# Optimization experiments

Hardware: AMD Instinct MI355X
Metric: run time of the kernel (lower is better)

## Reference

```python
import jax, jax.numpy as jnp
import numpy as np

NX, NY, NZ = 256, 256, 64
M = 400000
NFEATS = 16
OFFSETS = [(dx, dy, dz) for dx in (-1, 0, 1) for dy in (-1, 0, 1) for dz in (-1, 0, 1)]


def setup_inputs() -> dict:
    key = jax.random.key(0)
    ks = jax.random.split(key, 24)
    # unique active voxel sites (submanifold conv assumes unique active coords)
    flat = jax.random.permutation(ks[0], NX * NY * NZ)[:M]
    x = (flat // (NY * NZ)).astype(jnp.int32)
    y = ((flat // NZ) % NY).astype(jnp.int32)
    z = (flat % NZ).astype(jnp.int32)
    indices = jnp.stack([jnp.zeros_like(x), x, y, z], axis=-1)  # [M,4] = (batch,x,y,z)
    # dense grid -> row lookup (row+1, 0 means empty); this is the spconv rulebook analogue
    table = jnp.zeros(NX * NY * NZ, jnp.int32).at[flat].set(jnp.arange(M, dtype=jnp.int32) + 1)
    s = 0.05
    def w(k, shape):
        return jax.random.normal(ks[k], shape, jnp.float32) * s
    return {
        "features": jax.random.normal(ks[1], (M, NFEATS), jnp.float32),
        "w1": w(2, (27, NFEATS, 64)), "b1": w(3, (64,)),
        "w2": w(4, (27, 64, 64)), "b2": w(5, (64,)),
        "w3": w(6, (27, 64, 64)), "b3": w(7, (64,)),
        "cw11": w(8, (64, 64, 5, 5)), "cb11": w(9, (64,)),
        "cw12": w(10, (64, 64, 5, 5)), "cb12": w(11, (64,)),
        "cpw1": w(12, (64, 64, 1, 1)), "cpb1": w(13, (64,)),
        "cw21": w(14, (3, 64, 5, 5)), "cb21": w(15, (3,)),
        "cw22": w(16, (3, 3, 5, 5)), "cb22": w(17, (3,)),
        "cpw2": w(18, (3, 64, 1, 1)), "cpb2": w(19, (3,)),
        "indices": indices,
        "table": table,
    }


def subm_conv3d(feats, xyz, table, w, b):
    # submanifold 3x3x3 conv: outputs only at active sites, gathering active neighbors
    acc = jnp.zeros((feats.shape[0], w.shape[-1]), feats.dtype)
    for k, (dx, dy, dz) in enumerate(OFFSETS):
        nx, ny, nz = xyz[:, 0] + dx, xyz[:, 1] + dy, xyz[:, 2] + dz
        valid = (nx >= 0) & (nx < NX) & (ny >= 0) & (ny < NY) & (nz >= 0) & (nz < NZ)
        flat = jnp.clip(nx * (NY * NZ) + ny * NZ + nz, 0, NX * NY * NZ - 1)
        rows = table[flat]  # [M], 0 == empty
        ok = valid & (rows > 0)
        nf = feats[jnp.where(ok, rows - 1, 0)] * ok[:, None].astype(feats.dtype)
        acc = acc + nf @ w[k]  # gather-GEMM-accumulate
    return acc + b


def conv2d(x, w, b, pad):
    y = jax.lax.conv_general_dilated(x, w, (1, 1), [(pad, pad), (pad, pad)],
                                     dimension_numbers=("NCHW", "OIHW", "NCHW"))
    return y + b[None, :, None, None]


def resblock(x, w1, b1, w2, b2, pw, pb):
    h = jax.nn.relu(conv2d(x, w1, b1, 2))
    h = conv2d(h, w2, b2, 2)
    return jax.nn.relu(h + conv2d(x, pw, pb, 0))


def reference(features, w1, b1, w2, b2, w3, b3,
              cw11, cb11, cw12, cb12, cpw1, cpb1,
              cw21, cb21, cw22, cb22, cpw2, cpb2,
              indices, table):
    xyz = indices[:, 1:]
    h = jax.nn.relu(subm_conv3d(features, xyz, table, w1, b1))
    h = jax.nn.relu(subm_conv3d(h, xyz, table, w2, b2))
    h = subm_conv3d(h, xyz, table, w3, b3)
    # scatter-max voxel -> BEV over z (batch_size = 1)
    seg = indices[:, 1] * NY + indices[:, 2]
    bev = jax.ops.segment_max(h, seg, num_segments=NX * NY)
    bev = jnp.where(jnp.isneginf(bev), 0.0, bev)  # torch_scatter fills empty with 0
    bev = bev.reshape(1, NX, NY, 64).transpose(0, 3, 1, 2)  # NCHW
    out = resblock(bev, cw11, cb11, cw12, cb12, cpw1, cpb1)
    out = resblock(out, cw21, cb21, cw22, cb22, cpw2, cpb2)
    return out.transpose(0, 2, 3, 1)  # [1, NX, NY, 3]
```

## Files before the change

### kernel.cpp

```cpp
#include <hip/hip_runtime.h>
#include <math.h>

#define NXD 256
#define NYD 256
#define NZD 64
#define NCELL (NXD*NYD)

typedef __bf16 bf16x8 __attribute__((ext_vector_type(8)));
typedef float f32x4 __attribute__((ext_vector_type(4)));

__global__ __launch_bounds__(64) void zero_k(int* p) { p[threadIdx.x] = 0; }

__global__ __launch_bounds__(256) void f2bf_k(const float* __restrict__ in,
                                              __bf16* __restrict__ out, int n) {
    int i = blockIdx.x * 256 + threadIdx.x;
    if (i < n) out[i] = (__bf16)in[i];
}

__global__ __launch_bounds__(256) void count_k(const int* __restrict__ table,
                                               int* __restrict__ partial) {
    __shared__ int red[4];
    int tid = threadIdx.x, lane = tid & 63, wid = tid >> 6;
    int4 v = *(const int4*)(table + blockIdx.x * 1024 + tid * 4);
    int c = (v.x > 0) + (v.y > 0) + (v.z > 0) + (v.w > 0);
    for (int d = 32; d; d >>= 1) c += __shfl_down(c, d, 64);
    if (lane == 0) red[wid] = c;
    __syncthreads();
    if (tid == 0) partial[blockIdx.x] = red[0] + red[1] + red[2] + red[3];
}

__global__ __launch_bounds__(1024) void scan_k(const int* __restrict__ partial,
                                               int* __restrict__ scanned) {
    __shared__ int wsum[16];
    int tid = threadIdx.x, lane = tid & 63, wid = tid >> 6;
    int4 v = ((const int4*)partial)[tid];
    int tot = v.x + v.y + v.z + v.w;
    int sc = tot;
    for (int d = 1; d < 64; d <<= 1) { int o = __shfl_up(sc, d, 64); if (lane >= d) sc += o; }
    if (lane == 63) wsum[wid] = sc;
    __syncthreads();
    int wbase = 0;
    for (int w = 0; w < 16; ++w) if (w < wid) wbase += wsum[w];
    int excl = wbase + sc - tot;
    int4 o4;
    o4.x = excl; o4.y = excl + v.x; o4.z = excl + v.x + v.y; o4.w = excl + v.x + v.y + v.z;
    ((int4*)scanned)[tid] = o4;
}

__global__ __launch_bounds__(256) void emit_k(const int* __restrict__ table,
        const int* __restrict__ scanned, int* __restrict__ table2,
        int* __restrict__ perm, int4* __restrict__ coords) {
    __shared__ int wsum[4];
    int tid = threadIdx.x, lane = tid & 63, wid = tid >> 6;
    int gbase = blockIdx.x * 1024 + tid * 4;
    int4 v = *(const int4*)(table + gbase);
    int vals[4] = {v.x, v.y, v.z, v.w};
    int c = (v.x > 0) + (v.y > 0) + (v.z > 0) + (v.w > 0);
    int sc = c;
    for (int d = 1; d < 64; d <<= 1) { int o = __shfl_up(sc, d, 64); if (lane >= d) sc += o; }
    if (lane == 63) wsum[wid] = sc;
    __syncthreads();
    int wbase = 0;
    for (int w = 0; w < 4; ++w) if (w < wid) wbase += wsum[w];
    int pos = scanned[blockIdx.x] + wbase + sc - c;
    int t2[4];
    #pragma unroll
    for (int j = 0; j < 4; ++j) {
        int flat = gbase + j;
        if (vals[j] > 0) {
            t2[j] = pos + 1;
            perm[pos] = vals[j] - 1;
            coords[pos] = make_int4(0, flat >> 14, (flat >> 6) & 255, flat & 63);
            ++pos;
        } else t2[j] = 0;
    }
    *(int4*)(table2 + gbase) = make_int4(t2[0], t2[1], t2[2], t2[3]);
}

__global__ __launch_bounds__(256) void remap_feat_k(const float* __restrict__ f,
        const int* __restrict__ perm, __bf16* __restrict__ out) {
    int p = blockIdx.x * 64 + (threadIdx.x >> 2);
    int j = threadIdx.x & 3;
    float4 v = ((const float4*)(f + (size_t)perm[p] * 16))[j];
    __bf16* dst = out + (size_t)p * 16 + j * 4;
    dst[0] = (__bf16)v.x; dst[1] = (__bf16)v.y; dst[2] = (__bf16)v.z; dst[3] = (__bf16)v.w;
}

template<int CIN, int KS>
__global__ __launch_bounds__(256) void frag_w_k(const float* __restrict__ w,
                                                __bf16* __restrict__ wtf) {
    int k = blockIdx.x;
    for (int idx = threadIdx.x; idx < 4 * KS * 512; idx += 256) {
        int j = idx & 7, l = (idx >> 3) & 63, f = idx >> 9;
        int ctg = f / KS, ks = f % KS;
        int co = ctg * 16 + (l & 15);
        int ci = ks * 32 + ((l >> 4) * 8) + j;
        float v = (ci < CIN) ? w[((size_t)k * CIN + ci) * 64 + co] : 0.f;
        wtf[((size_t)k * 4 * KS + f) * 512 + (idx & 511)] = (__bf16)v;
    }
}

template<int CO, int COPAD>
__global__ __launch_bounds__(256) void transpose_cw_k(const float* __restrict__ w,
                                                      __bf16* __restrict__ wt) {
    int k = blockIdx.x;
    for (int idx = threadIdx.x; idx < COPAD * 64; idx += 256) {
        int ci = idx & 63, co = idx >> 6;
        float v = (co < CO) ? w[((size_t)co * 64 + ci) * 25 + k] : 0.f;
        wt[((size_t)k * COPAD + co) * 64 + ci] = (__bf16)v;
    }
}

template<int CIN, bool RELU>
__global__ __launch_bounds__(256) void subm_mfma_k(
        const __bf16* __restrict__ feats,
        const int4* __restrict__ coords,
        const int* __restrict__ table,
        const __bf16* __restrict__ wtf,
        const float* __restrict__ bias,
        __bf16* __restrict__ outp,
        const __bf16* __restrict__ zp) {
    constexpr int KS = (CIN == 64) ? 2 : 1;
    __shared__ int rows_lds[128 * 33];

    const int tid = threadIdx.x, lane = tid & 63, wid = tid >> 6;
    const int ch = wid & 1, pg = wid >> 1;
    const int lr = lane & 15, lg = lane >> 4;
    const int p0 = blockIdx.x * 128;

    if (ch == 0) {
        int4 c4 = coords[p0 + pg * 64 + lane];
        const int px = c4.y, py = c4.z, pz = c4.w;
        #pragma unroll
        for (int k = 0; k < 27; ++k) {
            const int nx = px + k / 9 - 1, ny = py + (k / 3) % 3 - 1, nz = pz + k % 3 - 1;
            const bool v = ((unsigned)nx < NXD) & ((unsigned)ny < NYD) & ((unsigned)nz < NZD);
            rows_lds[(pg * 64 + lane) * 33 + k] = v ? table[(nx * NYD + ny) * NZD + nz] : 0;
        }
    }
    __syncthreads();

    f32x4 acc[4][2];
    #pragma unroll
    for (int ct = 0; ct < 2; ++ct) {
        float b = bias[ch * 32 + ct * 16 + lr];
        #pragma unroll
        for (int pt = 0; pt < 4; ++pt) acc[pt][ct] = f32x4{b, b, b, b};
    }

    auto RD = [&](int k, int (&r)[4]) {
        if (k < 27) {
            #pragma unroll
            for (int pt = 0; pt < 4; ++pt)
                r[pt] = rows_lds[(pg * 64 + pt * 16 + lr) * 33 + k];
        }
    };

    auto LOADK = [&](int k, bf16x8 (&a)[4][KS], bf16x8 (&w)[2][KS], int& sm,
                     const int (&rr)[4]) {
        #pragma unroll
        for (int ct = 0; ct < 2; ++ct)
            #pragma unroll
            for (int ks = 0; ks < KS; ++ks)
                w[ct][ks] = *(const bf16x8*)(wtf +
                    ((size_t)(k * 4 + ch * 2 + ct) * KS + ks) * 512 + lane * 8);
        sm = 0;
        #pragma unroll
        for (int pt = 0; pt < 4; ++pt) {
            int srow = rr[pt];
            unsigned long long bm = __ballot(srow != 0);
            if (bm) {
                sm |= 1 << pt;
                if (CIN == 64) {
                    const __bf16* ab = (srow > 0) ? feats + (size_t)(srow - 1) * 64 : zp;
                    #pragma unroll
                    for (int ks = 0; ks < KS; ++ks)
                        a[pt][ks] = *(const bf16x8*)(ab + ks * 32 + lg * 8);
                } else {
                    const __bf16* ab = (srow > 0 && lg < 2)
                        ? feats + (size_t)(srow - 1) * 16 + lg * 8 : zp;
                    a[pt][0] = *(const bf16x8*)ab;
                }
            }
        }
    };
    auto MMAK = [&](bf16x8 (&a)[4][KS], bf16x8 (&w)[2][KS], int sm) {
        __builtin_amdgcn_s_setprio(1);
        #pragma unroll
        for (int pt = 0; pt < 4; ++pt)
            if (sm & (1 << pt))
                #pragma unroll
                for (int ct = 0; ct < 2; ++ct)
                    #pragma unroll
                    for (int ks = 0; ks < KS; ++ks)
                        acc[pt][ct] = __builtin_amdgcn_mfma_f32_16x16x32_bf16(
                            a[pt][ks], w[ct][ks], acc[pt][ct], 0, 0, 0);
        __builtin_amdgcn_s_setprio(0);
    };

    bf16x8 aX[4][KS], wX[2][KS], aY[4][KS], wY[2][KS];
    int smX, smY;
    int rA[4], rB[4];
    RD(0, rA);
    RD(1, rB);
    LOADK(0, aX, wX, smX, rA);
    #pragma unroll 1
    for (int k = 0; k < 26; k += 2) {
        RD(k + 2, rA);
        LOADK(k + 1, aY, wY, smY, rB);
        MMAK(aX, wX, smX);
        RD(k + 3, rB);
        LOADK(k + 2, aX, wX, smX, rA);
        MMAK(aY, wY, smY);
    }
    MMAK(aX, wX, smX);

    #pragma unroll
    for (int pt = 0; pt < 4; ++pt)
        #pragma unroll
        for (int ct = 0; ct < 2; ++ct) {
            const int co = ch * 32 + ct * 16 + lr;
            #pragma unroll
            for (int r = 0; r < 4; ++r) {
                int p = p0 + pg * 64 + pt * 16 + lg * 4 + r;
                float v = acc[pt][ct][r];
                if (RELU) v = fmaxf(v, 0.f);
                outp[(size_t)p * 64 + co] = (__bf16)v;
            }
        }
}

__global__ __launch_bounds__(256) void bev_max_k(const __bf16* __restrict__ h,
        const int* __restrict__ table, __bf16* __restrict__ bev) {
    int cell = blockIdx.x * 4 + (threadIdx.x >> 6);
    int lane = threadIdx.x & 63;
    int r = table[cell * 64 + lane];
    float acc = -INFINITY;
    #pragma unroll 1
    for (int z = 0; z < 64; ++z) {
        int row = __shfl(r, z, 64);
        if (row > 0) acc = fmaxf(acc, (float)h[(size_t)(row - 1) * 64 + lane]);
    }
    bev[(size_t)cell * 64 + lane] = (__bf16)((acc == -INFINITY) ? 0.f : acc);
}

template<bool RELU, bool FUSE_PW>
__global__ __launch_bounds__(256) void conv5_mfma_k(
        const __bf16* __restrict__ in,
        const __bf16* __restrict__ wtc,
        const float* __restrict__ bias,
        const __bf16* __restrict__ xres,
        const __bf16* __restrict__ wpw,
        const float* __restrict__ bpw,
        __bf16* __restrict__ out) {
    __shared__ __bf16 halo[400 * 64];
    __shared__ __bf16 xt[256 * 64];

    const int tid = threadIdx.x;
    const int gx0 = (blockIdx.x & 15) * 16;
    const int gy0 = (blockIdx.x >> 4) * 16;

    for (int i = tid; i < 3200; i += 256) {
        int hp = i >> 3, ch = i & 7;
        int hy = hp / 20, hx = hp - hy * 20;
        int gy = gy0 - 2 + hy, gx = gx0 - 2 + hx;
        uint4 v = {0, 0, 0, 0};
        if (gy >= 0 && gy < NXD && gx >= 0 && gx < NYD)
            v = *(const uint4*)(in + (((size_t)(gy << 8) + gx) << 6) + ch * 8);
        *(uint4*)((char*)halo + hp * 128 + ((ch ^ (hp & 7)) << 4)) = v;
    }
    if (FUSE_PW) {
        for (int i = tid; i < 2048; i += 256) {
            int p = i >> 3, ch = i & 7;
            int gy = gy0 + (p >> 4), gx = gx0 + (p & 15);
            uint4 v = *(const uint4*)(xres + (((size_t)(gy << 8) + gx) << 6) + ch * 8);
            *(uint4*)((char*)xt + p * 128 + ((ch ^ (p & 7)) << 4)) = v;
        }
    }
    __syncthreads();

    const int lane = tid & 63, wid = tid >> 6;
    const int lr = lane & 15, lg = lane >> 4;
    const int co = wid * 16 + lr;

    f32x4 acc[16];
    {
        float b = bias[co] + (FUSE_PW ? bpw[co] : 0.f);
        #pragma unroll
        for (int pt = 0; pt < 16; ++pt) acc[pt] = f32x4{b, b, b, b};
    }

    #pragma unroll 1
    for (int k = 0; k < 25; ++k) {
        const int dy = k / 5, dx = k - dy * 5;
        const __bf16* wrow = wtc + ((size_t)k * 64 + co) * 64 + lg * 8;
        bf16x8 bf0 = *(const bf16x8*)wrow;
        bf16x8 bf1 = *(const bf16x8*)(wrow + 32);
        #pragma unroll
        for (int pt = 0; pt < 16; ++pt) {
            int hp = (pt + dy) * 20 + lr + dx;
            bf16x8 a0 = *(const bf16x8*)((char*)halo + hp * 128 + ((lg ^ (hp & 7)) << 4));
            bf16x8 a1 = *(const bf16x8*)((char*)halo + hp * 128 + (((4 + lg) ^ (hp & 7)) << 4));
            acc[pt] = __builtin_amdgcn_mfma_f32_16x16x32_bf16(a0, bf0, acc[pt], 0, 0, 0);
            acc[pt] = __builtin_amdgcn_mfma_f32_16x16x32_bf16(a1, bf1, acc[pt], 0, 0, 0);
        }
    }
    if (FUSE_PW) {
        const __bf16* wrow = wpw + (size_t)co * 64 + lg * 8;
        bf16x8 bf0 = *(const bf16x8*)wrow;
        bf16x8 bf1 = *(const bf16x8*)(wrow + 32);
        #pragma unroll
        for (int pt = 0; pt < 16; ++pt) {
            int p = pt * 16 + lr;
            bf16x8 a0 = *(const bf16x8*)((char*)xt + p * 128 + ((lg ^ (p & 7)) << 4));
            bf16x8 a1 = *(const bf16x8*)((char*)xt + p * 128 + (((4 + lg) ^ (p & 7)) << 4));
            acc[pt] = __builtin_amdgcn_mfma_f32_16x16x32_bf16(a0, bf0, acc[pt], 0, 0, 0);
            acc[pt] = __builtin_amdgcn_mfma_f32_16x16x32_bf16(a1, bf1, acc[pt], 0, 0, 0);
        }
    }

    #pragma unroll
    for (int pt = 0; pt < 16; ++pt) {
        int gy = gy0 + pt;
        #pragma unroll
        for (int r = 0; r < 4; ++r) {
            int gx = gx0 + lg * 4 + r;
            float v = acc[pt][r];
            if (RELU) v = fmaxf(v, 0.f);
            out[(((size_t)(gy << 8) + gx) << 6) + co] = (__bf16)v;
        }
    }
}

__global__ __launch_bounds__(256) void conv5_mfma3_k(
        const __bf16* __restrict__ in,
        const __bf16* __restrict__ wtc,
        const float* __restrict__ bias3,
        float* __restrict__ out) {
    __shared__ __bf16 halo[400 * 64];

    const int tid = threadIdx.x;
    const int gx0 = (blockIdx.x & 15) * 16;
    const int gy0 = (blockIdx.x >> 4) * 16;

    for (int i = tid; i < 3200; i += 256) {
        int hp = i >> 3, ch = i & 7;
        int hy = hp / 20, hx = hp - hy * 20;
        int gy = gy0 - 2 + hy, gx = gx0 - 2 + hx;
        uint4 v = {0, 0, 0, 0};
        if (gy >= 0 && gy < NXD && gx >= 0 && gx < NYD)
            v = *(const uint4*)(in + (((size_t)(gy << 8) + gx) << 6) + ch * 8);
        *(uint4*)((char*)halo + hp * 128 + ((ch ^ (hp & 7)) << 4)) = v;
    }
    __syncthreads();

    const int lane = tid & 63, wid = tid >> 6;
    const int lr = lane & 15, lg = lane >> 4;

    f32x4 acc[4];
    {
        float b = (lr < 3) ? bias3[lr] : 0.f;
        #pragma unroll
        for (int t = 0; t < 4; ++t) acc[t] = f32x4{b, b, b, b};
    }

    #pragma unroll 1
    for (int k = 0; k < 25; ++k) {
        const int dy = k / 5, dx = k - dy * 5;
        const __bf16* wrow = wtc + ((size_t)k * 16 + lr) * 64 + lg * 8;
        bf16x8 bf0 = *(const bf16x8*)wrow;
        bf16x8 bf1 = *(const bf16x8*)(wrow + 32);
        #pragma unroll
        for (int t = 0; t < 4; ++t) {
            int pt = wid * 4 + t;
            int hp = (pt + dy) * 20 + lr + dx;
            bf16x8 a0 = *(const bf16x8*)((char*)halo + hp * 128 + ((lg ^ (hp & 7)) << 4));
            bf16x8 a1 = *(const bf16x8*)((char*)halo + hp * 128 + (((4 + lg) ^ (hp & 7)) << 4));
            acc[t] = __builtin_amdgcn_mfma_f32_16x16x32_bf16(a0, bf0, acc[t], 0, 0, 0);
            acc[t] = __builtin_amdgcn_mfma_f32_16x16x32_bf16(a1, bf1, acc[t], 0, 0, 0);
        }
    }

    if (lr < 3) {
        #pragma unroll
        for (int t = 0; t < 4; ++t) {
            int gy = gy0 + wid * 4 + t;
            #pragma unroll
            for (int r = 0; r < 4; ++r) {
                int gx = gx0 + lg * 4 + r;
                out[(size_t)lr * NCELL + (gy << 8) + gx] = fmaxf(acc[t][r], 0.f);
            }
        }
    }
}

template<int CIN, int COB, bool RELU>
__global__ __launch_bounds__(256) void conv5_k(const float* __restrict__ in,
        const float* __restrict__ w, const float* __restrict__ bias,
        float* __restrict__ out) {
    __shared__ float tile[20][20];
    int tid = threadIdx.x;
    int tx = tid & 15, ty = tid >> 4;
    int gx0 = blockIdx.x * 16 - 2, gy0 = blockIdx.y * 16 - 2;
    int co_base = blockIdx.z * COB;
    float acc[COB];
    #pragma unroll
    for (int i = 0; i < COB; ++i) acc[i] = bias[co_base + i];

    #pragma unroll 1
    for (int ci = 0; ci < CIN; ++ci) {
        __syncthreads();
        for (int idx = tid; idx < 400; idx += 256) {
            int r = idx / 20, cc = idx % 20;
            int sy = gy0 + r, sx = gx0 + cc;
            float v = 0.f;
            if (sy >= 0 && sy < NXD && sx >= 0 && sx < NYD)
                v = in[(size_t)ci * NCELL + sy * NYD + sx];
            tile[r][cc] = v;
        }
        __syncthreads();
        const float* wrow = w + ((size_t)co_base * CIN + ci) * 25;
        #pragma unroll
        for (int dy = 0; dy < 5; ++dy)
        #pragma unroll
        for (int dx = 0; dx < 5; ++dx) {
            float iv = tile[ty + dy][tx + dx];
            #pragma unroll
            for (int co = 0; co < COB; ++co)
                acc[co] = fmaf(iv, wrow[(size_t)co * CIN * 25 + dy * 5 + dx], acc[co]);
        }
    }
    int gy = gy0 + 2 + ty, gx = gx0 + 2 + tx;
    #pragma unroll
    for (int co = 0; co < COB; ++co) {
        float v = acc[co];
        if (RELU) v = fmaxf(v, 0.f);
        out[(size_t)(co_base + co) * NCELL + gy * NYD + gx] = v;
    }
}

__global__ __launch_bounds__(256) void pw_final_k(const __bf16* __restrict__ x,
        const float* __restrict__ pw, const float* __restrict__ pb,
        const float* __restrict__ h2, float* __restrict__ out) {
    int pix = blockIdx.x * 256 + threadIdx.x;
    float acc[3];
    #pragma unroll
    for (int co = 0; co < 3; ++co) acc[co] = pb[co] + h2[(size_t)co * NCELL + pix];
    const bf16x8* xr = (const bf16x8*)(x + (size_t)pix * 64);
    #pragma unroll
    for (int j = 0; j < 8; ++j) {
        bf16x8 v8 = xr[j];
        #pragma unroll
        for (int e = 0; e < 8; ++e) {
            float v = (float)v8[e];
            int ci = j * 8 + e;
            #pragma unroll
            for (int co = 0; co < 3; ++co) acc[co] = fmaf(v, pw[co * 64 + ci], acc[co]);
        }
    }
    #pragma unroll
    for (int co = 0; co < 3; ++co) out[(size_t)pix * 3 + co] = fmaxf(acc[co], 0.f);
}

extern "C" void kernel_launch(void* const* d_in, const int* in_sizes, int n_in,
                              void* d_out, int out_size, void* d_ws, size_t ws_size,
                              hipStream_t stream) {
    const float* features = (const float*)d_in[0];
    const float* w1   = (const float*)d_in[1];
    const float* b1   = (const float*)d_in[2];
    const float* w2   = (const float*)d_in[3];
    const float* b2   = (const float*)d_in[4];
    const float* w3   = (const float*)d_in[5];
    const float* b3   = (const float*)d_in[6];
    const float* cw11 = (const float*)d_in[7];
    const float* cb11 = (const float*)d_in[8];
    const float* cw12 = (const float*)d_in[9];
    const float* cb12 = (const float*)d_in[10];
    const float* cpw1 = (const float*)d_in[11];
    const float* cpb1 = (const float*)d_in[12];
    const float* cw21 = (const float*)d_in[13];
    const float* cb21 = (const float*)d_in[14];
    const float* cw22 = (const float*)d_in[15];
    const float* cb22 = (const float*)d_in[16];
    const float* cpw2 = (const float*)d_in[17];
    const float* cpb2 = (const float*)d_in[18];
    const int* table   = (const int*)d_in[20];
    const int M = in_sizes[0] / 16;

    char* ws = (char*)d_ws;
    __bf16* A_bf    = (__bf16*)(ws);
    __bf16* B_bf    = (__bf16*)(ws +  51200000ull);
    __bf16* feat_s  = (__bf16*)(ws + 102400000ull);
    __bf16* C_bf    = (__bf16*)(ws + 102400000ull);
    int4*   coords  = (int4*)  (ws + 153600000ull);
    int*    table2  = (int*)   (ws + 160000000ull);
    int*    perm    = (int*)   (ws + 176777216ull);
    int*    partial = (int*)   (ws + 178377216ull);
    int*    scanned = (int*)   (ws + 178393600ull);
    __bf16* BEV     = (__bf16*)(ws + 204800000ull);
    __bf16* H1      = (__bf16*)(ws + 213188608ull);
    __bf16* T1      = (__bf16*)(ws + 221577216ull);
    float*  S1      = (float*) (ws + 229965824ull);
    float*  S2      = (float*) (ws + 230752256ull);
    __bf16* WTC11   = (__bf16*)(ws + 232534016ull);
    __bf16* WTC12   = (__bf16*)(ws + 232738816ull);
    __bf16* WTC21   = (__bf16*)(ws + 232943616ull);
    __bf16* WPW1    = (__bf16*)(ws + 232994816ull);
    __bf16* WTF1    = (__bf16*)(ws + 233003008ull);
    __bf16* WTF2    = (__bf16*)(ws + 233113600ull);
    __bf16* WTF3    = (__bf16*)(ws + 233334784ull);
    __bf16* ZP      = (__bf16*)(ws + 233555968ull);

    count_k<<<4096, 256, 0, stream>>>(table, partial);
    scan_k<<<1, 1024, 0, stream>>>(partial, scanned);
    emit_k<<<4096, 256, 0, stream>>>(table, scanned, table2, perm, coords);
    remap_feat_k<<<M / 64, 256, 0, stream>>>(features, perm, feat_s);

    zero_k<<<1, 64, 0, stream>>>((int*)ZP);
    f2bf_k<<<16, 256, 0, stream>>>(cpw1, WPW1, 4096);
    frag_w_k<16, 1><<<27, 256, 0, stream>>>(w1, WTF1);
    frag_w_k<64, 2><<<27, 256, 0, stream>>>(w2, WTF2);
    frag_w_k<64, 2><<<27, 256, 0, stream>>>(w3, WTF3);
    transpose_cw_k<64, 64><<<25, 256, 0, stream>>>(cw11, WTC11);
    transpose_cw_k<64, 64><<<25, 256, 0, stream>>>(cw12, WTC12);
    transpose_cw_k<3, 16><<<25, 256, 0, stream>>>(cw21, WTC21);

    const int pblocks = M / 128;
    subm_mfma_k<16, true ><<<pblocks, 256, 0, stream>>>(feat_s, coords, table2, WTF1, b1, A_bf, ZP);
    subm_mfma_k<64, true ><<<pblocks, 256, 0, stream>>>(A_bf,   coords, table2, WTF2, b2, B_bf, ZP);
    subm_mfma_k<64, false><<<pblocks, 256, 0, stream>>>(B_bf,   coords, table2, WTF3, b3, C_bf, ZP);

    bev_max_k<<<NCELL / 4, 256, 0, stream>>>(C_bf, table2, BEV);

    conv5_mfma_k<true, false><<<256, 256, 0, stream>>>(BEV, WTC11, cb11, nullptr, nullptr, nullptr, H1);
    conv5_mfma_k<true, true ><<<256, 256, 0, stream>>>(H1, WTC12, cb12, BEV, WPW1, cpb1, T1);

    conv5_mfma3_k<<<256, 256, 0, stream>>>(T1, WTC21, cb21, S1);
    conv5_k<3, 3, false><<<dim3(16, 16, 1), 256, 0, stream>>>(S1, cw22, cb22, S2);
    pw_final_k<<<NCELL / 256, 256, 0, stream>>>(T1, cpw2, cpb2, S2, (float*)d_out);
}
```

Measured before the change: 607.0 us.

## Pack two kernel offsets per MFMA in first submanifold conv layer

For the 16-channel first layer, each 32-wide MFMA K slice previously held 16 real channels and 16 zero-padded ones. The change packs two neighbor offsets into one K slice: lanes in groups 2-3 gather the second offset's row, and a new weight-fragment kernel interleaves weights to match, cutting the offset loop from 27 to 14 steps. The neighbor-row LDS layout is also transposed to offset-major with a zero 28th row to support the paired reads. The catch is that the active-tile mask now covers the union of two offsets, so a few MFMAs may still run on partly empty tiles.

```diff
diff --git a/kernel.cpp b/kernel.cpp
--- a/kernel.cpp
+++ b/kernel.cpp
@@ -100,6 +100,20 @@
     }
 }
 
+__global__ __launch_bounds__(256) void frag_w16p_k(const float* __restrict__ w,
+                                                   __bf16* __restrict__ wtf) {
+    int kp = blockIdx.x;
+    for (int idx = threadIdx.x; idx < 4 * 512; idx += 256) {
+        int j = idx & 7, l = (idx >> 3) & 63, f = idx >> 9;
+        int co = f * 16 + (l & 15);
+        int lg = l >> 4;
+        int k = 2 * kp + (lg >> 1);
+        int ci = (lg & 1) * 8 + j;
+        float v = (k < 27) ? w[((size_t)k * 16 + ci) * 64 + co] : 0.f;
+        wtf[((size_t)kp * 4 + f) * 512 + (idx & 511)] = (__bf16)v;
+    }
+}
+
 template<int CO, int COPAD>
 __global__ __launch_bounds__(256) void transpose_cw_k(const float* __restrict__ w,
                                                       __bf16* __restrict__ wt) {
@@ -121,7 +135,8 @@
         __bf16* __restrict__ outp,
         const __bf16* __restrict__ zp) {
     constexpr int KS = (CIN == 64) ? 2 : 1;
-    __shared__ int rows_lds[128 * 33];
+    constexpr int PH = (CIN == 64) ? 27 : 14;
+    __shared__ int rows_lds[28][128];
 
     const int tid = threadIdx.x, lane = tid & 63, wid = tid >> 6;
     const int ch = wid & 1, pg = wid >> 1;
@@ -135,8 +150,9 @@
         for (int k = 0; k < 27; ++k) {
             const int nx = px + k / 9 - 1, ny = py + (k / 3) % 3 - 1, nz = pz + k % 3 - 1;
             const bool v = ((unsigned)nx < NXD) & ((unsigned)ny < NYD) & ((unsigned)nz < NZD);
-            rows_lds[(pg * 64 + lane) * 33 + k] = v ? table[(nx * NYD + ny) * NZD + nz] : 0;
-        }
+            rows_lds[k][pg * 64 + lane] = v ? table[(nx * NYD + ny) * NZD + nz] : 0;
+        }
+        rows_lds[27][pg * 64 + lane] = 0;
     }
     __syncthreads();
 
@@ -148,22 +164,23 @@
         for (int pt = 0; pt < 4; ++pt) acc[pt][ct] = f32x4{b, b, b, b};
     }
 
-    auto RD = [&](int k, int (&r)[4]) {
-        if (k < 27) {
+    auto RD = [&](int p, int (&r)[4]) {
+        if (p < PH) {
+            const int kk = (CIN == 64) ? p : (2 * p + (lg >> 1));
             #pragma unroll
             for (int pt = 0; pt < 4; ++pt)
-                r[pt] = rows_lds[(pg * 64 + pt * 16 + lr) * 33 + k];
+                r[pt] = rows_lds[kk][pg * 64 + pt * 16 + lr];
         }
     };
 
-    auto LOADK = [&](int k, bf16x8 (&a)[4][KS], bf16x8 (&w)[2][KS], int& sm,
+    auto LOADK = [&](int p, bf16x8 (&a)[4][KS], bf16x8 (&w)[2][KS], int& sm,
                      const int (&rr)[4]) {
         #pragma unroll
         for (int ct = 0; ct < 2; ++ct)
             #pragma unroll
             for (int ks = 0; ks < KS; ++ks)
                 w[ct][ks] = *(const bf16x8*)(wtf +
-                    ((size_t)(k * 4 + ch * 2 + ct) * KS + ks) * 512 + lane * 8);
+                    ((size_t)(p * 4 + ch * 2 + ct) * KS + ks) * 512 + lane * 8);
         sm = 0;
         #pragma unroll
         for (int pt = 0; pt < 4; ++pt) {
@@ -177,8 +194,8 @@
                     for (int ks = 0; ks < KS; ++ks)
                         a[pt][ks] = *(const bf16x8*)(ab + ks * 32 + lg * 8);
                 } else {
-                    const __bf16* ab = (srow > 0 && lg < 2)
-                        ? feats + (size_t)(srow - 1) * 16 + lg * 8 : zp;
+                    const __bf16* ab = (srow > 0)
+                        ? feats + (size_t)(srow - 1) * 16 + (lg & 1) * 8 : zp;
                     a[pt][0] = *(const bf16x8*)ab;
                 }
             }
@@ -205,15 +222,21 @@
     RD(1, rB);
     LOADK(0, aX, wX, smX, rA);
     #pragma unroll 1
-    for (int k = 0; k < 26; k += 2) {
-        RD(k + 2, rA);
-        LOADK(k + 1, aY, wY, smY, rB);
+    for (int p = 0; p + 2 < PH; p += 2) {
+        RD(p + 2, rA);
+        LOADK(p + 1, aY, wY, smY, rB);
         MMAK(aX, wX, smX);
-        RD(k + 3, rB);
-        LOADK(k + 2, aX, wX, smX, rA);
+        RD(p + 3, rB);
+        LOADK(p + 2, aX, wX, smX, rA);
         MMAK(aY, wY, smY);
     }
-    MMAK(aX, wX, smX);
+    if constexpr (PH & 1) {
+        MMAK(aX, wX, smX);
+    } else {
+        LOADK(PH - 1, aY, wY, smY, rB);
+        MMAK(aX, wX, smX);
+        MMAK(aY, wY, smY);
+    }
 
     #pragma unroll
     for (int pt = 0; pt < 4; ++pt)
@@ -518,7 +541,7 @@
 
     zero_k<<<1, 64, 0, stream>>>((int*)ZP);
     f2bf_k<<<16, 256, 0, stream>>>(cpw1, WPW1, 4096);
-    frag_w_k<16, 1><<<27, 256, 0, stream>>>(w1, WTF1);
+    frag_w16p_k<<<14, 256, 0, stream>>>(w1, WTF1);
     frag_w_k<64, 2><<<27, 256, 0, stream>>>(w2, WTF2);
     frag_w_k<64, 2><<<27, 256, 0, stream>>>(w3, WTF3);
     transpose_cw_k<64, 64><<<25, 256, 0, stream>>>(cw11, WTC11);
```

Result: faster. 585.6 us (-3.5%).
